# Kernel tuning notes

Hardware: AMD Instinct MI355X
Metric: run time of the kernel (lower is better)

## Reference

```python
import jax, jax.numpy as jnp
import numpy as np

N = 16384      # points
F = 16         # input feature dim
ATT = 32       # attention_dim == d_model of positional encoding
NFREQ = 64     # num_freq_bands
MAXFREQ = 10.0
K = 32         # knn k
B = 8          # number of graphs in batch
FEAT_DIM = F + ATT   # 48
POS_DIM = 3 + ATT    # 35


def setup_inputs() -> dict:
    key = jax.random.key(0)
    ks = jax.random.split(key, 12)
    x = jax.random.normal(ks[0], (N, F), dtype=jnp.float32)
    pos = jax.random.normal(ks[1], (N, 3), dtype=jnp.float32) * 3.0
    batch = jnp.sort(jax.random.randint(ks[2], (N,), 0, B)).astype(jnp.int64)
    def lin(k1, k2, fin, fout):
        w = jax.random.normal(k1, (fin, fout), dtype=jnp.float32) / np.sqrt(fin)
        b = jax.random.normal(k2, (fout,), dtype=jnp.float32) * 0.01
        return w, b
    w1f, b1f = lin(ks[3], ks[4], FEAT_DIM, ATT)
    w2f, b2f = lin(ks[5], ks[6], ATT, 1)
    w1p, b1p = lin(ks[7], ks[8], POS_DIM, ATT)
    w2p, b2p = lin(ks[9], ks[10], ATT, 1)
    return {"x": x, "pos": pos, "batch": batch,
            "w1f": w1f, "b1f": b1f, "w2f": w2f, "b2f": b2f,
            "w1p": w1p, "b1p": b1p, "w2p": w2p, "b2p": b2p}


def _positional_encoding(xyz):
    # [N,3] -> [N, ATT]; sin/cos interleaved over linspace freq bands, truncated
    fb = jnp.linspace(1.0, MAXFREQ, NFREQ).astype(xyz.dtype)       # [NFREQ]
    xf = xyz[:, :, None] * fb                                      # [N,3,NFREQ]
    enc = jnp.stack([jnp.sin(xf), jnp.cos(xf)], axis=-1)           # [N,3,NFREQ,2]
    enc = enc.reshape(xyz.shape[0], -1)                            # [N, 3*NFREQ*2]
    return enc[:, :ATT]


def _combined_normalized(x, pos, batch, w1f, b1f, w2f, b2f, w1p, b1p, w2p, b2p):
    xyz = pos[:, :3]
    enc = _positional_encoding(xyz)
    feat = jnp.concatenate([x, enc], axis=-1)      # [N, FEAT_DIM]
    pe = jnp.concatenate([xyz, enc], axis=-1)      # [N, POS_DIM]
    # AdaptiveBlending: two tiny MLPs -> softmax over 2 logits
    fw = jnp.maximum(feat @ w1f + b1f, 0.0) @ w2f + b2f   # [N,1]
    pw = jnp.maximum(pe @ w1p + b1p, 0.0) @ w2p + b2p     # [N,1]
    sw = jax.nn.softmax(jnp.concatenate([fw, pw], axis=-1), axis=-1)  # [N,2]
    combined = jnp.concatenate([pe * sw[:, 1:2], feat * sw[:, 0:1]], axis=-1)  # [N, POS+FEAT]
    # batch_normalize: per-graph scatter mean / unbiased std (torch_scatter default)
    ones = jnp.ones((combined.shape[0],), combined.dtype)
    cnt = jax.ops.segment_sum(ones, batch, num_segments=B)[:, None]     # [B,1]
    s = jax.ops.segment_sum(combined, batch, num_segments=B)            # [B,D]
    mean = s / jnp.maximum(cnt, 1.0)
    ss = jax.ops.segment_sum(combined * combined, batch, num_segments=B)
    var = (ss - cnt * mean * mean) / jnp.maximum(cnt - 1.0, 1.0)
    std = jnp.sqrt(jnp.clip(var, 0.0))
    return (combined - mean[batch]) / (std[batch] + 1e-8)


def reference(x, pos, batch, w1f, b1f, w2f, b2f, w1p, b1p, w2p, b2p):
    z = _combined_normalized(x, pos, batch, w1f, b1f, w2f, b2f, w1p, b1p, w2p, b2p)
    # focal_points = all points; per-batch masked KNN over squared distances
    sq = jnp.sum(z * z, axis=-1)                                    # [N]
    d2 = sq[:, None] + sq[None, :] - 2.0 * (z @ z.T)                # [N,N]
    same = batch[:, None] == batch[None, :]
    d2 = jnp.where(same, d2, jnp.inf)
    _, idx = jax.lax.top_k(-d2, K)                                  # [N,K]
    row = jnp.repeat(jnp.arange(z.shape[0], dtype=jnp.int64), K)    # query index
    col = idx.reshape(-1).astype(jnp.int64)                         # neighbor index
    return row, col
```

## Files before the change

### kernel.cpp

```cpp
#include <hip/hip_runtime.h>
#include <math.h>

#define NPTS 16384
#define KNN 32
#define NB 8
#define CD 83
#define CDP 84
#define PDIM 35
#define QPB 8
#define NSL 16
#define MST 33

typedef unsigned long long ull;

__device__ __forceinline__ int bval(const int* __restrict__ p, int i, int is32) {
    return is32 ? p[i] : p[2 * i];
}

__device__ __forceinline__ ull distkey(float d, int idx) {
    unsigned u = __float_as_uint(d);
    u = (u & 0x80000000u) ? ~u : (u | 0x80000000u);
    return ((ull)u << 32) | (unsigned)idx;
}

__device__ __forceinline__ float np_sincos_f32(float x, int compute_cos) {
    const float two_over_pi = 0x1.45f306p-1f;
    const float c1 = -0x1.921fb0p+00f;
    const float c2 = -0x1.5110b4p-22f;
    const float c3 = -0x1.846988p-48f;
    const float rint_cvt = 12582912.0f;
    float q = __fsub_rn(__fadd_rn(__fmul_rn(x, two_over_pi), rint_cvt), rint_cvt);
    float rx = __builtin_fmaf(q, c1, x);
    rx = __builtin_fmaf(q, c2, rx);
    rx = __builtin_fmaf(q, c3, rx);
    float r2 = __fmul_rn(rx, rx);
    float yc = __builtin_fmaf(0x1.98e616p-16f, r2, -0x1.6c06dcp-10f);
    yc = __builtin_fmaf(yc, r2, 0x1.55553cp-05f);
    yc = __builtin_fmaf(yc, r2, -0x1.000000p-1f);
    yc = __builtin_fmaf(yc, r2, 0x1.000000p+0f);
    float ys = __builtin_fmaf(0x1.7d3bbcp-19f, r2, -0x1.a06bbap-13f);
    ys = __builtin_fmaf(ys, r2, 0x1.11119ap-07f);
    ys = __builtin_fmaf(ys, r2, -0x1.555556p-03f);
    ys = __fmul_rn(ys, r2);
    ys = __builtin_fmaf(ys, rx, rx);
    int iq = (int)q + compute_cos;
    float res = ((iq & 1) == 0) ? ys : yc;
    if (iq & 2) res = __int_as_float(__float_as_int(res) ^ 0x80000000u);
    return res;
}

__device__ __forceinline__ float np_exp_f32(float x) {
    const float log2e = 1.442695040f;
    const float rint_cvt = 12582912.0f;
    if (x < -87.33654f) return 0.0f;
    float q = __fsub_rn(__fadd_rn(__fmul_rn(x, log2e), rint_cvt), rint_cvt);
    float r = __builtin_fmaf(q, -0.693359375f, x);
    r = __builtin_fmaf(q, 2.12194440e-4f, r);
    float y = 1.9875691500e-4f;
    y = __builtin_fmaf(y, r, 1.3981999507e-3f);
    y = __builtin_fmaf(y, r, 8.3334519073e-3f);
    y = __builtin_fmaf(y, r, 4.1665795894e-2f);
    y = __builtin_fmaf(y, r, 1.6666665459e-1f);
    y = __builtin_fmaf(y, r, 5.0000001201e-1f);
    float r2 = __fmul_rn(r, r);
    y = __builtin_fmaf(y, r2, r);
    y = __fadd_rn(y, 1.0f);
    int iq = (int)q;
    float sc = __int_as_float((127 + iq) << 23);
    return __fmul_rn(y, sc);
}

__device__ __forceinline__ float np_gemv32(const float* h, const float* __restrict__ w) {
    float a0 = 0.f, a1 = 0.f, a2 = 0.f, a3 = 0.f, a4 = 0.f, a5 = 0.f, a6 = 0.f, a7 = 0.f;
    #pragma unroll
    for (int t = 0; t < 32; t += 8) {
        a0 = __builtin_fmaf(h[t],     w[t],     a0);
        a1 = __builtin_fmaf(h[t + 1], w[t + 1], a1);
        a2 = __builtin_fmaf(h[t + 2], w[t + 2], a2);
        a3 = __builtin_fmaf(h[t + 3], w[t + 3], a3);
        a4 = __builtin_fmaf(h[t + 4], w[t + 4], a4);
        a5 = __builtin_fmaf(h[t + 5], w[t + 5], a5);
        a6 = __builtin_fmaf(h[t + 6], w[t + 6], a6);
        a7 = __builtin_fmaf(h[t + 7], w[t + 7], a7);
    }
    float s0 = __fadd_rn(a0, a4);
    float s1 = __fadd_rn(a1, a5);
    float s2 = __fadd_rn(a2, a6);
    float s3 = __fadd_rn(a3, a7);
    return __fadd_rn(__fadd_rn(s0, s1), __fadd_rn(s2, s3));
}

__global__ void k_flag(const int* __restrict__ batch32, int* __restrict__ flag) {
    if (threadIdx.x == 0) flag[0] = (batch32[NPTS - 1] != 0) ? 1 : 0;
}

__global__ void k_bounds(const int* __restrict__ batch, const int* __restrict__ flag,
                         int* __restrict__ seg) {
    int b = threadIdx.x;
    if (b > NB) return;
    int is32 = flag[0];
    int lo = 0, hi = NPTS;
    while (lo < hi) { int mid = (lo + hi) >> 1; if (bval(batch, mid, is32) < b) lo = mid + 1; else hi = mid; }
    seg[b] = lo;
}

__global__ void __launch_bounds__(256) k_front(
    const float* __restrict__ x, const float* __restrict__ pos,
    const float* __restrict__ w1f, const float* __restrict__ b1f,
    const float* __restrict__ w2f, const float* __restrict__ b2f,
    const float* __restrict__ w1p, const float* __restrict__ b1p,
    const float* __restrict__ w2p, const float* __restrict__ b2p,
    float* __restrict__ comb)
{
    __shared__ float s_w1f[48 * 32];
    __shared__ float s_w1p[35 * 32];
    __shared__ float s_b1f[32], s_w2f[32], s_b1p[32], s_w2p[32];
    __shared__ float s_b2[2];
    int t = threadIdx.x;
    for (int idx = t; idx < 48 * 32; idx += 256) s_w1f[idx] = w1f[idx];
    for (int idx = t; idx < 35 * 32; idx += 256) s_w1p[idx] = w1p[idx];
    if (t < 32) { s_b1f[t] = b1f[t]; s_w2f[t] = w2f[t]; s_b1p[t] = b1p[t]; s_w2p[t] = w2p[t]; }
    if (t == 0) { s_b2[0] = b2f[0]; s_b2[1] = b2p[0]; }
    __syncthreads();

    int i = blockIdx.x * 256 + t;

    float xr[16];
    const float4* x4 = (const float4*)(x + (long)i * 16);
    #pragma unroll
    for (int d4 = 0; d4 < 4; ++d4) {
        float4 v = x4[d4];
        xr[4 * d4] = v.x; xr[4 * d4 + 1] = v.y; xr[4 * d4 + 2] = v.z; xr[4 * d4 + 3] = v.w;
    }
    float p0 = pos[i * 3], p1 = pos[i * 3 + 1], p2 = pos[i * 3 + 2];

    float enc[32];
    #pragma unroll
    for (int f = 0; f < 16; ++f) {
        float fbf = (float)((double)f * (9.0 / 63.0) + 1.0);
        float a = __fmul_rn(p0, fbf);
        enc[2 * f] = np_sincos_f32(a, 0);
        enc[2 * f + 1] = np_sincos_f32(a, 1);
    }

    float h[32], hr[32];
    #pragma unroll
    for (int j = 0; j < 32; ++j) h[j] = 0.0f;
    #pragma unroll
    for (int k = 0; k < 16; ++k) {
        float v = xr[k];
        #pragma unroll
        for (int j = 0; j < 32; ++j) h[j] = __builtin_fmaf(v, s_w1f[k * 32 + j], h[j]);
    }
    for (int e = 0; e < 32; ++e) {
        float v = enc[e];
        #pragma unroll
        for (int j = 0; j < 32; ++j) h[j] = __builtin_fmaf(v, s_w1f[(16 + e) * 32 + j], h[j]);
    }
    #pragma unroll
    for (int j = 0; j < 32; ++j) hr[j] = fmaxf(__fadd_rn(h[j], s_b1f[j]), 0.0f);
    float fw = __fadd_rn(np_gemv32(hr, s_w2f), s_b2[0]);

    #pragma unroll
    for (int j = 0; j < 32; ++j) h[j] = 0.0f;
    {
        #pragma unroll
        for (int j = 0; j < 32; ++j) h[j] = __builtin_fmaf(p0, s_w1p[0 * 32 + j], h[j]);
        #pragma unroll
        for (int j = 0; j < 32; ++j) h[j] = __builtin_fmaf(p1, s_w1p[1 * 32 + j], h[j]);
        #pragma unroll
        for (int j = 0; j < 32; ++j) h[j] = __builtin_fmaf(p2, s_w1p[2 * 32 + j], h[j]);
    }
    for (int e = 0; e < 32; ++e) {
        float v = enc[e];
        #pragma unroll
        for (int j = 0; j < 32; ++j) h[j] = __builtin_fmaf(v, s_w1p[(3 + e) * 32 + j], h[j]);
    }
    #pragma unroll
    for (int j = 0; j < 32; ++j) hr[j] = fmaxf(__fadd_rn(h[j], s_b1p[j]), 0.0f);
    float pw = __fadd_rn(np_gemv32(hr, s_w2p), s_b2[1]);

    float m = fmaxf(fw, pw);
    float e0 = np_exp_f32(__fsub_rn(fw, m));
    float e1 = np_exp_f32(__fsub_rn(pw, m));
    float s = __fadd_rn(e0, e1);
    float sw0 = __fdiv_rn(e0, s);
    float sw1 = __fdiv_rn(e1, s);

    float* out = comb + (long)i * CDP;
    out[0] = __fmul_rn(p0, sw1);
    out[1] = __fmul_rn(p1, sw1);
    out[2] = __fmul_rn(p2, sw1);
    #pragma unroll
    for (int e = 0; e < 32; ++e) out[3 + e] = __fmul_rn(enc[e], sw1);
    #pragma unroll
    for (int k = 0; k < 16; ++k) out[35 + k] = __fmul_rn(xr[k], sw0);
    #pragma unroll
    for (int e = 0; e < 32; ++e) out[51 + e] = __fmul_rn(enc[e], sw0);
    out[83] = 0.0f;
}

__global__ void __launch_bounds__(128) k_stats(
    const float* __restrict__ comb, const int* __restrict__ seg,
    float* __restrict__ meanb, float* __restrict__ denb)
{
    int b = blockIdx.x;
    int d = threadIdx.x;
    if (d >= CD) return;
    int start = seg[b], end = seg[b + 1];
    float sum = 0.0f, ss = 0.0f;
    int r = start;
    for (; r + 8 <= end; r += 8) {
        float v0 = comb[(long)(r + 0) * CDP + d];
        float v1 = comb[(long)(r + 1) * CDP + d];
        float v2 = comb[(long)(r + 2) * CDP + d];
        float v3 = comb[(long)(r + 3) * CDP + d];
        float v4 = comb[(long)(r + 4) * CDP + d];
        float v5 = comb[(long)(r + 5) * CDP + d];
        float v6 = comb[(long)(r + 6) * CDP + d];
        float v7 = comb[(long)(r + 7) * CDP + d];
        sum = __fadd_rn(sum, v0); ss = __fadd_rn(ss, __fmul_rn(v0, v0));
        sum = __fadd_rn(sum, v1); ss = __fadd_rn(ss, __fmul_rn(v1, v1));
        sum = __fadd_rn(sum, v2); ss = __fadd_rn(ss, __fmul_rn(v2, v2));
        sum = __fadd_rn(sum, v3); ss = __fadd_rn(ss, __fmul_rn(v3, v3));
        sum = __fadd_rn(sum, v4); ss = __fadd_rn(ss, __fmul_rn(v4, v4));
        sum = __fadd_rn(sum, v5); ss = __fadd_rn(ss, __fmul_rn(v5, v5));
        sum = __fadd_rn(sum, v6); ss = __fadd_rn(ss, __fmul_rn(v6, v6));
        sum = __fadd_rn(sum, v7); ss = __fadd_rn(ss, __fmul_rn(v7, v7));
    }
    for (; r < end; ++r) {
        float c = comb[(long)r * CDP + d];
        sum = __fadd_rn(sum, c);
        ss = __fadd_rn(ss, __fmul_rn(c, c));
    }
    float cnt = (float)(end - start);
    float mn = __fdiv_rn(sum, fmaxf(cnt, 1.0f));
    float num = __fsub_rn(ss, __fmul_rn(__fmul_rn(cnt, mn), mn));
    float var = __fdiv_rn(num, fmaxf(__fsub_rn(cnt, 1.0f), 1.0f));
    if (var < 0.0f) var = 0.0f;
    meanb[b * CD + d] = mn;
    denb[b * CD + d] = __fadd_rn(__fsqrt_rn(var), 1e-8f);
}

__global__ void __launch_bounds__(256) k_z(
    float* __restrict__ comb, const int* __restrict__ batch, const int* __restrict__ flag,
    const float* __restrict__ meanb, const float* __restrict__ denb,
    float* __restrict__ sqb)
{
    int r = blockIdx.x * 256 + threadIdx.x;
    int b = bval(batch, r, flag[0]);
    const float* mb = meanb + b * CD;
    const float* db = denb + b * CD;
    float4* row4 = (float4*)(comb + (long)r * CDP);
    float rv[CDP];
    #pragma unroll
    for (int d4 = 0; d4 < 21; ++d4) {
        float4 v = row4[d4];
        rv[4 * d4] = v.x; rv[4 * d4 + 1] = v.y; rv[4 * d4 + 2] = v.z; rv[4 * d4 + 3] = v.w;
    }
    float p[CD];
    for (int d = 0; d < CD; ++d) {
        float zz = __fdiv_rn(__fsub_rn(rv[d], mb[d]), db[d]);
        rv[d] = zz;
        p[d] = __fmul_rn(zz, zz);
    }
    rv[83] = 0.0f;
    #pragma unroll
    for (int d4 = 0; d4 < 21; ++d4) {
        float4 v;
        v.x = rv[4 * d4]; v.y = rv[4 * d4 + 1]; v.z = rv[4 * d4 + 2]; v.w = rv[4 * d4 + 3];
        row4[d4] = v;
    }
    float r0 = p[0], r1 = p[1], r2 = p[2], r3 = p[3];
    float r4 = p[4], r5 = p[5], r6 = p[6], r7 = p[7];
    #pragma unroll
    for (int i = 8; i < 80; i += 8) {
        r0 = __fadd_rn(r0, p[i]);     r1 = __fadd_rn(r1, p[i + 1]);
        r2 = __fadd_rn(r2, p[i + 2]); r3 = __fadd_rn(r3, p[i + 3]);
        r4 = __fadd_rn(r4, p[i + 4]); r5 = __fadd_rn(r5, p[i + 5]);
        r6 = __fadd_rn(r6, p[i + 6]); r7 = __fadd_rn(r7, p[i + 7]);
    }
    float res = __fadd_rn(__fadd_rn(__fadd_rn(r0, r1), __fadd_rn(r2, r3)),
                          __fadd_rn(__fadd_rn(r4, r5), __fadd_rn(r6, r7)));
    res = __fadd_rn(res, p[80]);
    res = __fadd_rn(res, p[81]);
    res = __fadd_rn(res, p[82]);
    sqb[r] = res;
}

__global__ void __launch_bounds__(128) k_knn(
    const float* __restrict__ z, const float* __restrict__ sqb,
    const int* __restrict__ batch, const int* __restrict__ flag,
    const int* __restrict__ seg, int* __restrict__ out)
{
    __shared__ ull s_kl[64 * MST];

    int t = threadIdx.x;
    int q = t >> 4, s = t & 15;
    int i = blockIdx.x * QPB + q;
    int is32 = flag[0];
    int bi = bval(batch, i, is32);
    int lo = seg[bi], hi = seg[bi + 1];

    float zq[CDP];
    const float4* z4 = (const float4*)(z + (long)i * CDP);
    #pragma unroll
    for (int d4 = 0; d4 < 21; ++d4) {
        float4 v = z4[d4];
        zq[4 * d4] = v.x; zq[4 * d4 + 1] = v.y; zq[4 * d4 + 2] = v.z; zq[4 * d4 + 3] = v.w;
    }
    float sqi = sqb[i];

    ull kl[KNN];
    #pragma unroll
    for (int k = 0; k < KNN; ++k) kl[k] = ~0ull;

    for (int j = lo + s; j < hi; j += NSL) {
        const float4* zj4 = (const float4*)(z + (long)j * CDP);
        float sqj = sqb[j];
        float acc = 0.0f;
        #pragma unroll
        for (int d4 = 0; d4 < 21; ++d4) {
            float4 v = zj4[d4];
            acc = __builtin_fmaf(zq[4 * d4],     v.x, acc);
            acc = __builtin_fmaf(zq[4 * d4 + 1], v.y, acc);
            acc = __builtin_fmaf(zq[4 * d4 + 2], v.z, acc);
            acc = __builtin_fmaf(zq[4 * d4 + 3], v.w, acc);
        }
        float dist = __fsub_rn(__fadd_rn(sqi, sqj), __fmul_rn(2.0f, acc));
        ull key = distkey(dist, j);
        if (key < kl[KNN - 1]) {
            kl[KNN - 1] = key;
            #pragma unroll
            for (int k = KNN - 2; k >= 0; --k) {
                if (kl[k + 1] < kl[k]) { ull tmp = kl[k]; kl[k] = kl[k + 1]; kl[k + 1] = tmp; }
            }
        }
    }

    int* orow = out;
    int* ocol = out + (long)NPTS * KNN;
    #pragma unroll
    for (int half = 0; half < 2; ++half) {
        __syncthreads();
        if ((t >> 6) == half) {
            int qh = q & 3;
            #pragma unroll
            for (int k = 0; k < KNN; ++k) s_kl[(s * 4 + qh) * MST + k] = kl[k];
        }
        __syncthreads();
        if ((t >> 6) == half && s == 0) {
            int qh = q & 3;
            int p[NSL];
            #pragma unroll
            for (int l = 0; l < NSL; ++l) p[l] = 0;
            for (int k = 0; k < KNN; ++k) {
                ull best = ~0ull; int bl = 0;
                #pragma unroll
                for (int l = 0; l < NSL; ++l) {
                    int pp = p[l];
                    ull v = (pp < KNN) ? s_kl[(l * 4 + qh) * MST + pp] : ~0ull;
                    if (v < best) { best = v; bl = l; }
                }
                #pragma unroll
                for (int l = 0; l < NSL; ++l) if (bl == l) p[l]++;
                orow[(long)i * KNN + k] = i;
                ocol[(long)i * KNN + k] = (int)(best & 0xffffffffull);
            }
        }
    }
}

extern "C" void kernel_launch(void* const* d_in, const int* in_sizes, int n_in,
                              void* d_out, int out_size, void* d_ws, size_t ws_size,
                              hipStream_t stream)
{
    const float* x   = (const float*)d_in[0];
    const float* pos = (const float*)d_in[1];
    const int* batch = (const int*)d_in[2];
    const float* w1f = (const float*)d_in[3];
    const float* b1f = (const float*)d_in[4];
    const float* w2f = (const float*)d_in[5];
    const float* b2f = (const float*)d_in[6];
    const float* w1p = (const float*)d_in[7];
    const float* b1p = (const float*)d_in[8];
    const float* w2p = (const float*)d_in[9];
    const float* b2p = (const float*)d_in[10];

    char* ws = (char*)d_ws;
    float* comb  = (float*)(ws);
    float* sqb   = (float*)(ws + 5505024);
    float* meanb = (float*)(ws + 5570560);
    float* denb  = (float*)(ws + 5573216);
    int*   seg   = (int*)  (ws + 5575936);
    int*   flag  = (int*)  (ws + 5576000);
    int* out = (int*)d_out;

    hipLaunchKernelGGL(k_flag, dim3(1), dim3(64), 0, stream, batch, flag);
    hipLaunchKernelGGL(k_bounds, dim3(1), dim3(16), 0, stream, batch, flag, seg);
    hipLaunchKernelGGL(k_front, dim3(NPTS / 256), dim3(256), 0, stream,
                       x, pos, w1f, b1f, w2f, b2f, w1p, b1p, w2p, b2p, comb);
    hipLaunchKernelGGL(k_stats, dim3(NB), dim3(128), 0, stream, comb, seg, meanb, denb);
    hipLaunchKernelGGL(k_z, dim3(NPTS / 256), dim3(256), 0, stream, comb, batch, flag, meanb, denb, sqb);
    hipLaunchKernelGGL(k_knn, dim3(NPTS / QPB), dim3(128), 0, stream, comb, sqb, batch, flag, seg, out);
}
```

Measured before the change: 932.2 us.

## Rebalance KNN work split, unroll candidate loop by two, single-pass merge

The KNN kernel now gives each block 16 queries with 8 lanes each instead of 8 queries with 16 lanes. This halves the number of partial top-K lists that must be merged per query. The candidate loop handles two neighbors per iteration with independent accumulators to expose more instruction-level parallelism. Partial lists are stored as split 32-bit hi/lo arrays in shared memory so all queries merge in one pass instead of two halves. The launch bound is raised to 2 blocks per CU, which adds register pressure from the extra accumulators and loads alongside the 32-entry key list.

```diff
diff --git a/kernel.cpp b/kernel.cpp
--- a/kernel.cpp
+++ b/kernel.cpp
@@ -7,8 +7,8 @@
 #define CD 83
 #define CDP 84
 #define PDIM 35
-#define QPB 8
-#define NSL 16
+#define QPB 16
+#define NSL 8
 #define MST 33
 
 typedef unsigned long long ull;
@@ -288,15 +288,26 @@
     sqb[r] = res;
 }
 
-__global__ void __launch_bounds__(128) k_knn(
+__device__ __forceinline__ void insert_key(ull* kl, ull key) {
+    if (key < kl[KNN - 1]) {
+        kl[KNN - 1] = key;
+        #pragma unroll
+        for (int k = KNN - 2; k >= 0; --k) {
+            if (kl[k + 1] < kl[k]) { ull tmp = kl[k]; kl[k] = kl[k + 1]; kl[k + 1] = tmp; }
+        }
+    }
+}
+
+__global__ void __launch_bounds__(128, 2) k_knn(
     const float* __restrict__ z, const float* __restrict__ sqb,
     const int* __restrict__ batch, const int* __restrict__ flag,
     const int* __restrict__ seg, int* __restrict__ out)
 {
-    __shared__ ull s_kl[64 * MST];
+    __shared__ unsigned s_hi[128 * MST];
+    __shared__ unsigned s_lo[128 * MST];
 
     int t = threadIdx.x;
-    int q = t >> 4, s = t & 15;
+    int q = t >> 3, s = t & 7;
     int i = blockIdx.x * QPB + q;
     int is32 = flag[0];
     int bi = bval(batch, i, is32);
@@ -315,58 +326,79 @@
     #pragma unroll
     for (int k = 0; k < KNN; ++k) kl[k] = ~0ull;
 
-    for (int j = lo + s; j < hi; j += NSL) {
-        const float4* zj4 = (const float4*)(z + (long)j * CDP);
-        float sqj = sqb[j];
-        float acc = 0.0f;
+    int j = lo + s;
+    for (; j + NSL < hi; j += 2 * NSL) {
+        int j2 = j + NSL;
+        const float4* a4 = (const float4*)(z + (long)j * CDP);
+        const float4* b4 = (const float4*)(z + (long)j2 * CDP);
+        float sqa = sqb[j], sqc = sqb[j2];
+        float acc1 = 0.0f, acc2 = 0.0f;
         #pragma unroll
         for (int d4 = 0; d4 < 21; ++d4) {
-            float4 v = zj4[d4];
-            acc = __builtin_fmaf(zq[4 * d4],     v.x, acc);
-            acc = __builtin_fmaf(zq[4 * d4 + 1], v.y, acc);
-            acc = __builtin_fmaf(zq[4 * d4 + 2], v.z, acc);
-            acc = __builtin_fmaf(zq[4 * d4 + 3], v.w, acc);
+            float4 va = a4[d4];
+            float4 vb = b4[d4];
+            float q0 = zq[4 * d4], q1 = zq[4 * d4 + 1], q2 = zq[4 * d4 + 2], q3 = zq[4 * d4 + 3];
+            acc1 = __builtin_fmaf(q0, va.x, acc1);
+            acc2 = __builtin_fmaf(q0, vb.x, acc2);
+            acc1 = __builtin_fmaf(q1, va.y, acc1);
+            acc2 = __builtin_fmaf(q1, vb.y, acc2);
+            acc1 = __builtin_fmaf(q2, va.z, acc1);
+            acc2 = __builtin_fmaf(q2, vb.z, acc2);
+            acc1 = __builtin_fmaf(q3, va.w, acc1);
+            acc2 = __builtin_fmaf(q3, vb.w, acc2);
         }
-        float dist = __fsub_rn(__fadd_rn(sqi, sqj), __fmul_rn(2.0f, acc));
-        ull key = distkey(dist, j);
-        if (key < kl[KNN - 1]) {
-            kl[KNN - 1] = key;
+        float dist1 = __fsub_rn(__fadd_rn(sqi, sqa), __fmul_rn(2.0f, acc1));
+        float dist2 = __fsub_rn(__fadd_rn(sqi, sqc), __fmul_rn(2.0f, acc2));
+        insert_key(kl, distkey(dist1, j));
+        insert_key(kl, distkey(dist2, j2));
+    }
+    if (j < hi) {
+        const float4* a4 = (const float4*)(z + (long)j * CDP);
+        float sqa = sqb[j];
+        float acc1 = 0.0f;
+        #pragma unroll
+        for (int d4 = 0; d4 < 21; ++d4) {
+            float4 va = a4[d4];
+            acc1 = __builtin_fmaf(zq[4 * d4],     va.x, acc1);
+            acc1 = __builtin_fmaf(zq[4 * d4 + 1], va.y, acc1);
+            acc1 = __builtin_fmaf(zq[4 * d4 + 2], va.z, acc1);
+            acc1 = __builtin_fmaf(zq[4 * d4 + 3], va.w, acc1);
+        }
+        float dist1 = __fsub_rn(__fadd_rn(sqi, sqa), __fmul_rn(2.0f, acc1));
+        insert_key(kl, distkey(dist1, j));
+    }
+
+    #pragma unroll
+    for (int k = 0; k < KNN; ++k) {
+        ull v = kl[k];
+        s_hi[t * MST + k] = (unsigned)(v >> 32);
+        s_lo[t * MST + k] = (unsigned)(v & 0xffffffffull);
+    }
+    __syncthreads();
+
+    if (s == 0) {
+        int base = t;
+        int p[NSL];
+        #pragma unroll
+        for (int l = 0; l < NSL; ++l) p[l] = 0;
+        int* orow = out;
+        int* ocol = out + (long)NPTS * KNN;
+        for (int k = 0; k < KNN; ++k) {
+            ull best = ~0ull; int bl = 0;
             #pragma unroll
-            for (int k = KNN - 2; k >= 0; --k) {
-                if (kl[k + 1] < kl[k]) { ull tmp = kl[k]; kl[k] = kl[k + 1]; kl[k + 1] = tmp; }
+            for (int l = 0; l < NSL; ++l) {
+                int pp = p[l];
+                ull v = ~0ull;
+                if (pp < KNN) {
+                    int idx = (base + l) * MST + pp;
+                    v = ((ull)s_hi[idx] << 32) | s_lo[idx];
+                }
+                if (v < best) { best = v; bl = l; }
             }
-        }
-    }
-
-    int* orow = out;
-    int* ocol = out + (long)NPTS * KNN;
-    #pragma unroll
-    for (int half = 0; half < 2; ++half) {
-        __syncthreads();
-        if ((t >> 6) == half) {
-            int qh = q & 3;
             #pragma unroll
-            for (int k = 0; k < KNN; ++k) s_kl[(s * 4 + qh) * MST + k] = kl[k];
-        }
-        __syncthreads();
-        if ((t >> 6) == half && s == 0) {
-            int qh = q & 3;
-            int p[NSL];
-            #pragma unroll
-            for (int l = 0; l < NSL; ++l) p[l] = 0;
-            for (int k = 0; k < KNN; ++k) {
-                ull best = ~0ull; int bl = 0;
-                #pragma unroll
-                for (int l = 0; l < NSL; ++l) {
-                    int pp = p[l];
-                    ull v = (pp < KNN) ? s_kl[(l * 4 + qh) * MST + pp] : ~0ull;
-                    if (v < best) { best = v; bl = l; }
-                }
-                #pragma unroll
-                for (int l = 0; l < NSL; ++l) if (bl == l) p[l]++;
-                orow[(long)i * KNN + k] = i;
-                ocol[(long)i * KNN + k] = (int)(best & 0xffffffffull);
-            }
+            for (int l = 0; l < NSL; ++l) if (bl == l) p[l]++;
+            orow[(long)i * KNN + k] = i;
+            ocol[(long)i * KNN + k] = (int)(best & 0xffffffffull);
         }
     }
 }
```

After: 989.6 us. +6.2%, slower.
